# Kernel optimization log

Hardware: AMD Instinct MI355X
Metric: run time of the kernel (lower is better)

## Reference

```python
import jax, jax.numpy as jnp
import numpy as np

N = 100000
E = 1600000
D_IN = 128
D_OUT = 128
NEG_SLOPE = 0.01  # PyTorch LeakyReLU default


def setup_inputs() -> dict:
    key = jax.random.key(0)
    ks = jax.random.split(key, 6)
    x = jax.random.normal(ks[0], (N, D_IN), dtype=jnp.float32)
    src = jax.random.randint(ks[1], (E,), 0, N, dtype=jnp.int32)
    dst = jax.random.randint(ks[2], (E,), 0, N, dtype=jnp.int32)
    e_attn = jax.random.uniform(ks[3], (E,), dtype=jnp.float32)
    # Xavier-normal-ish init for linear weights
    std = float(np.sqrt(2.0 / (D_IN + D_OUT)))
    W1 = jax.random.normal(ks[4], (D_OUT, D_IN), dtype=jnp.float32) * std
    W2 = jax.random.normal(ks[5], (D_OUT, D_IN), dtype=jnp.float32) * std
    b1 = jnp.zeros((D_OUT,), dtype=jnp.float32)
    b2 = jnp.zeros((D_OUT,), dtype=jnp.float32)
    return {"x": x, "src": src, "dst": dst, "e_attn": e_attn,
            "W1": W1, "b1": b1, "W2": W2, "b2": b2}


def leaky_relu(v):
    return jnp.where(v >= 0, v, NEG_SLOPE * v)


def reference(x, src, dst, e_attn, W1, b1, W2, b2):
    # Edge-weighted gather-scatter: h_n[d] = sum_{e: dst(e)=d} a_e * x[src(e)]
    msgs = x[src] * e_attn[:, None]                      # [E, D_IN]
    h_n = jax.ops.segment_sum(msgs, dst, num_segments=N)  # [N, D_IN]
    # Bi-interaction: LeakyReLU(W1(x + h_n)) + LeakyReLU(W2(x * h_n))
    add_part = leaky_relu(jnp.einsum('nd,od->no', x + h_n, W1) + b1)
    mul_part = leaky_relu(jnp.einsum('nd,od->no', x * h_n, W2) + b2)
    return add_part + mul_part  # dropout p=0.0 -> identity
```

## Files before the change

### kernel.cpp

```cpp
#include <hip/hip_runtime.h>

#define N_NODES 100000
#define E_EDGES 1600000
#define D 128
#define AP 132
#define ASTR 136

typedef short s16x8 __attribute__((ext_vector_type(8)));
typedef unsigned short u16x8 __attribute__((ext_vector_type(8)));
typedef float f32x4 __attribute__((ext_vector_type(4)));

__device__ __forceinline__ unsigned short f2bf(float f) {
    union { float f; unsigned u; } v;
    v.f = f;
    unsigned r = v.u + 0x7FFFu + ((v.u >> 16) & 1u);
    return (unsigned short)(r >> 16);
}

__device__ __forceinline__ float bf2f(unsigned short u) {
    union { unsigned u; float f; } v;
    v.u = ((unsigned)u) << 16;
    return v.f;
}

__device__ __forceinline__ float lrelu(float v) {
    return v >= 0.0f ? v : 0.01f * v;
}

__global__ __launch_bounds__(256) void prep_kernel(
    const int* __restrict__ dst, const int* __restrict__ src,
    const float* __restrict__ ea,
    int* __restrict__ cnt, int stride,
    unsigned char* __restrict__ rank, int2* __restrict__ bucket, int cap,
    const float* __restrict__ x, unsigned short* __restrict__ xbf, int do_xconv,
    const float* __restrict__ W1, const float* __restrict__ W2,
    unsigned short* __restrict__ Wswz) {
    int b = blockIdx.x;
    int t = threadIdx.x;
    if (b < 6250) {
        int e = b * 256 + t;
        int d = dst[e];
        if (cap) {
            int s = src[e];
            float a = ea[e];
            int r = atomicAdd(&cnt[(size_t)d * stride], 1);
            if (r < cap) bucket[(size_t)d * cap + r] = make_int2(s, __float_as_int(a));
        } else {
            rank[e] = (unsigned char)atomicAdd(&cnt[(size_t)d * stride], 1);
        }
    } else if (b < 12500) {
        if (!do_xconv) return;
        int idx = (b - 6250) * 256 + t;
        const float4* xp = (const float4*)(x) + (size_t)idx * 2;
        float4 a = xp[0], bb = xp[1];
        u16x8 o;
        o[0] = f2bf(a.x);  o[1] = f2bf(a.y);  o[2] = f2bf(a.z);  o[3] = f2bf(a.w);
        o[4] = f2bf(bb.x); o[5] = f2bf(bb.y); o[6] = f2bf(bb.z); o[7] = f2bf(bb.w);
        ((u16x8*)(xbf))[idx] = o;
    } else {
        int tid = (b - 12500) * 256 + t;
        if (tid >= 2 * 4 * 8 * 64) return;
        int lane = tid & 63;
        int ct   = (tid >> 6) & 7;
        int ks   = (tid >> 9) & 3;
        int mat  = tid >> 11;
        const float* W = mat ? W2 : W1;
        int o  = ct * 16 + (lane & 15);
        int k0 = ks * 32 + (lane >> 4) * 8;
        const float* sp = W + (size_t)o * D + k0;
        u16x8 w;
#pragma unroll
        for (int j = 0; j < 8; ++j) w[j] = f2bf(sp[j]);
        ((u16x8*)(Wswz))[tid] = w;
    }
}

__global__ __launch_bounds__(256) void scanA_kernel(
    const int* __restrict__ cnt, int* __restrict__ excl,
    int* __restrict__ bsum, int n, int stride) {
    __shared__ int tmp[256];
    int gid = blockIdx.x * 256 + threadIdx.x;
    int v = (gid < n) ? cnt[(size_t)gid * stride] : 0;
    tmp[threadIdx.x] = v;
    __syncthreads();
    for (int ofs = 1; ofs < 256; ofs <<= 1) {
        int t = (threadIdx.x >= ofs) ? tmp[threadIdx.x - ofs] : 0;
        __syncthreads();
        tmp[threadIdx.x] += t;
        __syncthreads();
    }
    int incl = tmp[threadIdx.x];
    if (gid < n) excl[gid] = incl - v;
    if (threadIdx.x == 255) bsum[blockIdx.x] = incl;
}

__global__ __launch_bounds__(512) void scanB_kernel(int* __restrict__ bsum, int nb) {
    __shared__ int tmp[512];
    int v = (threadIdx.x < nb) ? bsum[threadIdx.x] : 0;
    tmp[threadIdx.x] = v;
    __syncthreads();
    for (int ofs = 1; ofs < 512; ofs <<= 1) {
        int t = (threadIdx.x >= ofs) ? tmp[threadIdx.x - ofs] : 0;
        __syncthreads();
        tmp[threadIdx.x] += t;
        __syncthreads();
    }
    if (threadIdx.x < nb) bsum[threadIdx.x] = tmp[threadIdx.x] - v;
}

__global__ __launch_bounds__(256) void fillC_kernel(
    const int* __restrict__ src, const int* __restrict__ dst,
    const float* __restrict__ ea, const int* __restrict__ excl,
    const int* __restrict__ bsum, const unsigned char* __restrict__ rank,
    int2* __restrict__ csr, int* __restrict__ off) {
    int gid = blockIdx.x * 256 + threadIdx.x;
    int d = dst[gid];
    int pos = excl[d] + bsum[d >> 8] + (int)rank[gid];
    csr[pos] = make_int2(src[gid], __float_as_int(ea[gid]));
    if (gid < N_NODES) off[gid] = excl[gid] + bsum[gid >> 8];
    else if (gid == N_NODES) off[N_NODES] = E_EDGES;
}

template <bool PADDED>
__global__ __launch_bounds__(256, 4) void fused_gg_kernel(
    const unsigned short* __restrict__ xbf, const int2* __restrict__ csr,
    const int* __restrict__ offc, int stride, int cap,
    const unsigned short* __restrict__ Wswz,
    const float* __restrict__ b1, const float* __restrict__ b2,
    float* __restrict__ out) {
    __shared__ unsigned short A[2][64 * ASTR];

    const int n0 = blockIdx.x * 64;
    const int t = threadIdx.x;
    const int lane = t & 63;
    const int wv = t >> 6;
    const int q = lane >> 4;
    const int li = lane & 15;

    for (int j = 0; j < 16; ++j) {
        const int row = wv * 16 + j;
        const int node = n0 + row;
        int beg = 0, end = 0;
        if (node < N_NODES) {
            if (PADDED) {
                beg = node * cap;
                int c = offc[(size_t)node * stride];
                end = beg + (c < cap ? c : cap);
            } else {
                beg = offc[node];
                end = offc[node + 1];
            }
        }

        float a0[8], a1[8];
#pragma unroll
        for (int d = 0; d < 8; ++d) { a0[d] = 0.f; a1[d] = 0.f; }

        int i = beg + q;
        for (; i + 4 < end; i += 8) {
            int2 p0 = csr[i];
            int2 p1 = csr[i + 4];
            float w0 = __int_as_float(p0.y);
            float w1 = __int_as_float(p1.y);
            u16x8 v0 = ((const u16x8*)(xbf + (size_t)p0.x * D))[li];
            u16x8 v1 = ((const u16x8*)(xbf + (size_t)p1.x * D))[li];
#pragma unroll
            for (int d = 0; d < 8; ++d) {
                a0[d] += w0 * bf2f(v0[d]);
                a1[d] += w1 * bf2f(v1[d]);
            }
        }
        if (i < end) {
            int2 p0 = csr[i];
            float w0 = __int_as_float(p0.y);
            u16x8 v0 = ((const u16x8*)(xbf + (size_t)p0.x * D))[li];
#pragma unroll
            for (int d = 0; d < 8; ++d) a0[d] += w0 * bf2f(v0[d]);
        }
#pragma unroll
        for (int d = 0; d < 8; ++d) a0[d] += a1[d];
#pragma unroll
        for (int d = 0; d < 8; ++d) a0[d] += __shfl_xor(a0[d], 16);
#pragma unroll
        for (int d = 0; d < 8; ++d) a0[d] += __shfl_xor(a0[d], 32);

        const int srcrow = node < N_NODES ? node : N_NODES - 1;
        if (q < 2) {
            u16x8 xu = ((const u16x8*)(xbf + (size_t)srcrow * D))[li];
            u16x8 o;
#pragma unroll
            for (int dd = 0; dd < 8; ++dd) {
                float xv = bf2f(xu[dd]);
                o[dd] = f2bf(q == 0 ? xv + a0[dd] : xv * a0[dd]);
            }
            *(u16x8*)&A[q][row * ASTR + li * 8] = o;
        }
    }

    s16x8 Bf[2][2][4];
    float bb1[2], bb2[2];
#pragma unroll
    for (int ci = 0; ci < 2; ++ci) {
        int ct = wv + ci * 4;
        bb1[ci] = b1[ct * 16 + li];
        bb2[ci] = b2[ct * 16 + li];
#pragma unroll
        for (int mat = 0; mat < 2; ++mat)
#pragma unroll
            for (int ks = 0; ks < 4; ++ks)
                Bf[ci][mat][ks] = *(const s16x8*)(
                    Wswz + ((size_t)(((mat * 4 + ks) * 8 + ct) * 64 + lane)) * 8);
    }

    __syncthreads();

    const int kq = q * 8;
#pragma unroll
    for (int mt = 0; mt < 4; ++mt) {
        f32x4 acc[2][2];
#pragma unroll
        for (int ci = 0; ci < 2; ++ci)
#pragma unroll
            for (int p = 0; p < 2; ++p) acc[ci][p] = (f32x4){0.f, 0.f, 0.f, 0.f};

        const int arow = mt * 16 + li;
#pragma unroll
        for (int ks = 0; ks < 4; ++ks) {
            s16x8 aa0 = *(const s16x8*)&A[0][arow * ASTR + ks * 32 + kq];
            s16x8 aa1 = *(const s16x8*)&A[1][arow * ASTR + ks * 32 + kq];
#pragma unroll
            for (int ci = 0; ci < 2; ++ci) {
                acc[ci][0] = __builtin_amdgcn_mfma_f32_16x16x32_bf16(
                    aa0, Bf[ci][0][ks], acc[ci][0], 0, 0, 0);
                acc[ci][1] = __builtin_amdgcn_mfma_f32_16x16x32_bf16(
                    aa1, Bf[ci][1][ks], acc[ci][1], 0, 0, 0);
            }
        }

#pragma unroll
        for (int ci = 0; ci < 2; ++ci) {
            int oc = (wv + ci * 4) * 16 + li;
#pragma unroll
            for (int r = 0; r < 4; ++r) {
                int node = n0 + mt * 16 + q * 4 + r;
                if (node < N_NODES) {
                    float v = lrelu(acc[ci][0][r] + bb1[ci])
                            + lrelu(acc[ci][1][r] + bb2[ci]);
                    out[(size_t)node * D + oc] = v;
                }
            }
        }
    }
}

__global__ __launch_bounds__(256) void gather_f32_kernel(
    const float* __restrict__ x, const int2* __restrict__ csr,
    const int* __restrict__ off, float* __restrict__ h) {
    int node = blockIdx.x * 4 + (threadIdx.x >> 6);
    int lane = threadIdx.x & 63;
    int beg = off[node];
    int end = off[node + 1];
    float2 acc0 = make_float2(0.f, 0.f);
    float2 acc1 = make_float2(0.f, 0.f);
    int e = beg;
    for (; e + 1 < end; e += 2) {
        int2 p0 = csr[e];
        int2 p1 = csr[e + 1];
        float a0 = __int_as_float(p0.y);
        float a1 = __int_as_float(p1.y);
        float2 v0 = ((const float2*)(x + (size_t)p0.x * D))[lane];
        float2 v1 = ((const float2*)(x + (size_t)p1.x * D))[lane];
        acc0.x += a0 * v0.x; acc0.y += a0 * v0.y;
        acc1.x += a1 * v1.x; acc1.y += a1 * v1.y;
    }
    if (e < end) {
        int2 p0 = csr[e];
        float a0 = __int_as_float(p0.y);
        float2 v0 = ((const float2*)(x + (size_t)p0.x * D))[lane];
        acc0.x += a0 * v0.x; acc0.y += a0 * v0.y;
    }
    acc0.x += acc1.x; acc0.y += acc1.y;
    ((float2*)(h + (size_t)node * D))[lane] = acc0;
}

__global__ __launch_bounds__(256, 4) void mfma_gemm_t1_kernel(
    const float* __restrict__ xf, const float* __restrict__ h,
    const unsigned short* __restrict__ Wswz,
    const float* __restrict__ b1, const float* __restrict__ b2,
    float* __restrict__ out) {
    __shared__ unsigned short A[2][64 * ASTR];
    const int n0 = blockIdx.x * 64;
    const int t = threadIdx.x;
    const int lane = t & 63;
    const int wv = t >> 6;
#pragma unroll
    for (int i = 0; i < 8; ++i) {
        int s = t + i * 256;
        int row = s >> 5;
        int c4 = s & 31;
        int srcrow = n0 + row;
        if (srcrow >= N_NODES) srcrow = N_NODES - 1;
        float4 xv = ((const float4*)(xf + (size_t)srcrow * D))[c4];
        float4 hv = ((const float4*)(h + (size_t)srcrow * D))[c4];
        ushort4 av, mv;
        av.x = f2bf(xv.x + hv.x); av.y = f2bf(xv.y + hv.y);
        av.z = f2bf(xv.z + hv.z); av.w = f2bf(xv.w + hv.w);
        mv.x = f2bf(xv.x * hv.x); mv.y = f2bf(xv.y * hv.y);
        mv.z = f2bf(xv.z * hv.z); mv.w = f2bf(xv.w * hv.w);
        *(ushort4*)&A[0][row * ASTR + c4 * 4] = av;
        *(ushort4*)&A[1][row * ASTR + c4 * 4] = mv;
    }
    s16x8 Bf[2][2][4];
    float bb1[2], bb2[2];
#pragma unroll
    for (int ci = 0; ci < 2; ++ci) {
        int ct = wv + ci * 4;
        bb1[ci] = b1[ct * 16 + (lane & 15)];
        bb2[ci] = b2[ct * 16 + (lane & 15)];
#pragma unroll
        for (int mat = 0; mat < 2; ++mat)
#pragma unroll
            for (int ks = 0; ks < 4; ++ks)
                Bf[ci][mat][ks] = *(const s16x8*)(
                    Wswz + ((size_t)(((mat * 4 + ks) * 8 + ct) * 64 + lane)) * 8);
    }
    __syncthreads();
    const int quad = lane >> 4;
    const int kq = quad * 8;
#pragma unroll
    for (int mt = 0; mt < 4; ++mt) {
        f32x4 acc[2][2];
#pragma unroll
        for (int ci = 0; ci < 2; ++ci)
#pragma unroll
            for (int p = 0; p < 2; ++p) acc[ci][p] = (f32x4){0.f, 0.f, 0.f, 0.f};
        const int arow = mt * 16 + (lane & 15);
#pragma unroll
        for (int ks = 0; ks < 4; ++ks) {
            s16x8 aa0 = *(const s16x8*)&A[0][arow * ASTR + ks * 32 + kq];
            s16x8 aa1 = *(const s16x8*)&A[1][arow * ASTR + ks * 32 + kq];
#pragma unroll
            for (int ci = 0; ci < 2; ++ci) {
                acc[ci][0] = __builtin_amdgcn_mfma_f32_16x16x32_bf16(
                    aa0, Bf[ci][0][ks], acc[ci][0], 0, 0, 0);
                acc[ci][1] = __builtin_amdgcn_mfma_f32_16x16x32_bf16(
                    aa1, Bf[ci][1][ks], acc[ci][1], 0, 0, 0);
            }
        }
#pragma unroll
        for (int ci = 0; ci < 2; ++ci) {
            int oc = (wv + ci * 4) * 16 + (lane & 15);
#pragma unroll
            for (int r = 0; r < 4; ++r) {
                int node = n0 + mt * 16 + quad * 4 + r;
                if (node < N_NODES) {
                    float v = lrelu(acc[ci][0][r] + bb1[ci])
                            + lrelu(acc[ci][1][r] + bb2[ci]);
                    out[(size_t)node * D + oc] = v;
                }
            }
        }
    }
}

__global__ __launch_bounds__(256) void scatter_kernel(
    const float* __restrict__ x, const int* __restrict__ src,
    const int* __restrict__ dst, const float* __restrict__ ea,
    float* __restrict__ h, int E) {
    int idx = blockIdx.x * 256 + threadIdx.x;
    int e = idx >> 5;
    int lane = idx & 31;
    if (e >= E) return;
    int s = src[e];
    int d = dst[e];
    float a = ea[e];
    float4 v = ((const float4*)(x + (size_t)s * D))[lane];
    float* hp = h + (size_t)d * D + lane * 4;
    atomicAdd(hp + 0, a * v.x);
    atomicAdd(hp + 1, a * v.y);
    atomicAdd(hp + 2, a * v.z);
    atomicAdd(hp + 3, a * v.w);
}

__global__ __launch_bounds__(256) void gemm_kernel(
    const float* __restrict__ x, const float* __restrict__ h,
    const float* __restrict__ W1, const float* __restrict__ b1,
    const float* __restrict__ W2, const float* __restrict__ b2,
    float* __restrict__ out) {
    __shared__ float Aadd[32 * AP];
    __shared__ float Amul[32 * AP];
    const int n0 = blockIdx.x * 32;
    const int t = threadIdx.x;
#pragma unroll
    for (int i = 0; i < 4; ++i) {
        int fi = t + i * 256;
        int row = fi >> 5;
        int c4 = fi & 31;
        float4 xv = ((const float4*)(x + (size_t)(n0 + row) * D))[c4];
        float4 hv = ((const float4*)(h + (size_t)(n0 + row) * D))[c4];
        float4 av = make_float4(xv.x + hv.x, xv.y + hv.y, xv.z + hv.z, xv.w + hv.w);
        float4 mv = make_float4(xv.x * hv.x, xv.y * hv.y, xv.z * hv.z, xv.w * hv.w);
        *((float4*)&Aadd[row * AP + c4 * 4]) = av;
        *((float4*)&Amul[row * AP + c4 * 4]) = mv;
    }
    __syncthreads();
    const int m0 = (t >> 5) * 4;
    const int o0 = (t & 31) * 4;
    float acc1[4][4];
    float acc2[4][4];
#pragma unroll
    for (int i = 0; i < 4; ++i)
#pragma unroll
        for (int j = 0; j < 4; ++j) { acc1[i][j] = 0.0f; acc2[i][j] = 0.0f; }
#pragma unroll 4
    for (int d = 0; d < D; d += 4) {
        float4 a[4], m[4], w1[4], w2[4];
#pragma unroll
        for (int i = 0; i < 4; ++i) a[i] = *(const float4*)&Aadd[(m0 + i) * AP + d];
#pragma unroll
        for (int i = 0; i < 4; ++i) m[i] = *(const float4*)&Amul[(m0 + i) * AP + d];
#pragma unroll
        for (int j = 0; j < 4; ++j) w1[j] = *(const float4*)&W1[(size_t)(o0 + j) * D + d];
#pragma unroll
        for (int j = 0; j < 4; ++j) w2[j] = *(const float4*)&W2[(size_t)(o0 + j) * D + d];
#pragma unroll
        for (int i = 0; i < 4; ++i)
#pragma unroll
            for (int j = 0; j < 4; ++j) {
                acc1[i][j] += a[i].x * w1[j].x + a[i].y * w1[j].y
                            + a[i].z * w1[j].z + a[i].w * w1[j].w;
                acc2[i][j] += m[i].x * w2[j].x + m[i].y * w2[j].y
                            + m[i].z * w2[j].z + m[i].w * w2[j].w;
            }
    }
#pragma unroll
    for (int i = 0; i < 4; ++i) {
        float4 r;
        float v1, v2;
        v1 = lrelu(acc1[i][0] + b1[o0 + 0]); v2 = lrelu(acc2[i][0] + b2[o0 + 0]); r.x = v1 + v2;
        v1 = lrelu(acc1[i][1] + b1[o0 + 1]); v2 = lrelu(acc2[i][1] + b2[o0 + 1]); r.y = v1 + v2;
        v1 = lrelu(acc1[i][2] + b1[o0 + 2]); v2 = lrelu(acc2[i][2] + b2[o0 + 2]); r.z = v1 + v2;
        v1 = lrelu(acc1[i][3] + b1[o0 + 3]); v2 = lrelu(acc2[i][3] + b2[o0 + 3]); r.w = v1 + v2;
        ((float4*)(out + (size_t)(n0 + m0 + i) * D))[t & 31] = r;
    }
}

extern "C" void kernel_launch(void* const* d_in, const int* in_sizes, int n_in,
                              void* d_out, int out_size, void* d_ws, size_t ws_size,
                              hipStream_t stream) {
    const float* x   = (const float*)d_in[0];
    const int*   src = (const int*)d_in[1];
    const int*   dst = (const int*)d_in[2];
    const float* ea  = (const float*)d_in[3];
    const float* W1  = (const float*)d_in[4];
    const float* b1  = (const float*)d_in[5];
    const float* W2  = (const float*)d_in[6];
    const float* b2  = (const float*)d_in[7];
    float* out = (float*)d_out;
    char* ws = (char*)d_ws;

    auto align256 = [](size_t v) { return (v + 255) & ~(size_t)255; };

    const size_t SZ_WSWZ = 2 * 4 * 8 * 64 * 8 * sizeof(unsigned short);
    const size_t SZ_OFF  = (size_t)(N_NODES + 1) * sizeof(int);
    const size_t SZ_EXCL = (size_t)N_NODES * sizeof(int);
    const size_t SZ_BSUM = 512 * sizeof(int);
    const size_t SZ_RANK = (size_t)E_EDGES;
    const size_t SZ_CSR  = (size_t)E_EDGES * sizeof(int2);
    const size_t SZ_XBF  = (size_t)N_NODES * D * sizeof(unsigned short);

    const int NB_E = 6250;
    const int NB_N = (N_NODES + 255) / 256;
    const int GB   = (N_NODES + 63) / 64;

    auto try_direct = [&](int cap) -> bool {
        size_t sz_cnt = (size_t)N_NODES * 16 * sizeof(int);
        size_t o_cnt  = align256(SZ_WSWZ);
        size_t o_bkt  = o_cnt + align256(sz_cnt);
        size_t o_xbf  = o_bkt + align256((size_t)N_NODES * cap * sizeof(int2));
        size_t need   = o_xbf + align256(SZ_XBF);
        if (ws_size < need) return false;
        unsigned short* Wswz = (unsigned short*)ws;
        int*  cnt = (int*)(ws + o_cnt);
        int2* bkt = (int2*)(ws + o_bkt);
        unsigned short* xbf = (unsigned short*)(ws + o_xbf);
        hipMemsetAsync(cnt, 0, sz_cnt, stream);
        prep_kernel<<<12516, 256, 0, stream>>>(dst, src, ea, cnt, 16,
                                               nullptr, bkt, cap,
                                               x, xbf, 1, W1, W2, Wswz);
        fused_gg_kernel<true><<<GB, 256, 0, stream>>>(xbf, bkt, cnt, 16, cap,
                                                      Wswz, b1, b2, out);
        return true;
    };
    if (try_direct(64)) return;
    if (try_direct(48)) return;

    auto try_exact = [&](int stride) -> bool {
        size_t sz_cnt = (size_t)N_NODES * stride * sizeof(int);
        size_t o_cnt  = align256(SZ_WSWZ);
        size_t o_off  = o_cnt + align256(sz_cnt);
        size_t o_excl = o_off + align256(SZ_OFF);
        size_t o_bsum = o_excl + align256(SZ_EXCL);
        size_t o_rank = o_bsum + align256(SZ_BSUM);
        size_t o_csr  = o_rank + align256(SZ_RANK);
        size_t o_xbf  = o_csr + align256(SZ_CSR);
        size_t need   = o_xbf + align256(SZ_XBF);
        if (ws_size < need) return false;
        unsigned short* Wswz = (unsigned short*)ws;
        int*  cnt  = (int*)(ws + o_cnt);
        int*  off  = (int*)(ws + o_off);
        int*  excl = (int*)(ws + o_excl);
        int*  bsum = (int*)(ws + o_bsum);
        unsigned char* rank = (unsigned char*)(ws + o_rank);
        int2* csr  = (int2*)(ws + o_csr);
        unsigned short* xbf = (unsigned short*)(ws + o_xbf);
        hipMemsetAsync(cnt, 0, sz_cnt, stream);
        prep_kernel<<<12516, 256, 0, stream>>>(dst, src, ea, cnt, stride,
                                               rank, nullptr, 0,
                                               x, xbf, 1, W1, W2, Wswz);
        scanA_kernel<<<NB_N, 256, 0, stream>>>(cnt, excl, bsum, N_NODES, stride);
        scanB_kernel<<<1, 512, 0, stream>>>(bsum, NB_N);
        fillC_kernel<<<NB_E, 256, 0, stream>>>(src, dst, ea, excl, bsum, rank,
                                               csr, off);
        fused_gg_kernel<false><<<GB, 256, 0, stream>>>(xbf, csr, off, 0, 0,
                                                       Wswz, b1, b2, out);
        return true;
    };
    if (try_exact(16)) return;
    if (try_exact(1)) return;

    {
        size_t sz_cnt = (size_t)N_NODES * sizeof(int);
        size_t o_cnt  = align256(SZ_WSWZ);
        size_t o_off  = o_cnt + align256(sz_cnt);
        size_t o_excl = o_off + align256(SZ_OFF);
        size_t o_bsum = o_excl + align256(SZ_EXCL);
        size_t o_rank = o_bsum + align256(SZ_BSUM);
        size_t o_csr  = o_rank + align256(SZ_RANK);
        size_t need   = o_csr + align256(SZ_CSR);
        if (ws_size >= need) {
            unsigned short* Wswz = (unsigned short*)ws;
            int*  cnt  = (int*)(ws + o_cnt);
            int*  off  = (int*)(ws + o_off);
            int*  excl = (int*)(ws + o_excl);
            int*  bsum = (int*)(ws + o_bsum);
            unsigned char* rank = (unsigned char*)(ws + o_rank);
            int2* csr  = (int2*)(ws + o_csr);
            hipMemsetAsync(cnt, 0, sz_cnt, stream);
            prep_kernel<<<12516, 256, 0, stream>>>(dst, src, ea, cnt, 1,
                                                   rank, nullptr, 0,
                                                   x, nullptr, 0, W1, W2, Wswz);
            scanA_kernel<<<NB_N, 256, 0, stream>>>(cnt, excl, bsum, N_NODES, 1);
            scanB_kernel<<<1, 512, 0, stream>>>(bsum, NB_N);
            fillC_kernel<<<NB_E, 256, 0, stream>>>(src, dst, ea, excl, bsum, rank,
                                                   csr, off);
            float* h = out;
            gather_f32_kernel<<<N_NODES / 4, 256, 0, stream>>>(x, csr, off, h);
            mfma_gemm_t1_kernel<<<GB, 256, 0, stream>>>(x, h, Wswz, b1, b2, out);
            return;
        }
    }

    {
        float* h = out;
        hipMemsetAsync(h, 0, (size_t)N_NODES * D * sizeof(float), stream);
        int total = E_EDGES * 32;
        scatter_kernel<<<(total + 255) / 256, 256, 0, stream>>>(x, src, dst, ea,
                                                                h, E_EDGES);
        gemm_kernel<<<N_NODES / 32, 256, 0, stream>>>(x, h, W1, b1, W2, b2, out);
    }
}
```

Baseline: 311.9 us.

## Drop padded-bucket direct path, use exact CSR with 4-way unrolled gather

```diff
diff --git a/kernel.cpp b/kernel.cpp
--- a/kernel.cpp
+++ b/kernel.cpp
@@ -28,10 +28,8 @@
 }
 
 __global__ __launch_bounds__(256) void prep_kernel(
-    const int* __restrict__ dst, const int* __restrict__ src,
-    const float* __restrict__ ea,
-    int* __restrict__ cnt, int stride,
-    unsigned char* __restrict__ rank, int2* __restrict__ bucket, int cap,
+    const int* __restrict__ dst, int* __restrict__ cnt,
+    unsigned char* __restrict__ rank, int stride,
     const float* __restrict__ x, unsigned short* __restrict__ xbf, int do_xconv,
     const float* __restrict__ W1, const float* __restrict__ W2,
     unsigned short* __restrict__ Wswz) {
@@ -39,15 +37,7 @@
     int t = threadIdx.x;
     if (b < 6250) {
         int e = b * 256 + t;
-        int d = dst[e];
-        if (cap) {
-            int s = src[e];
-            float a = ea[e];
-            int r = atomicAdd(&cnt[(size_t)d * stride], 1);
-            if (r < cap) bucket[(size_t)d * cap + r] = make_int2(s, __float_as_int(a));
-        } else {
-            rank[e] = (unsigned char)atomicAdd(&cnt[(size_t)d * stride], 1);
-        }
+        rank[e] = (unsigned char)atomicAdd(&cnt[(size_t)dst[e] * stride], 1);
     } else if (b < 12500) {
         if (!do_xconv) return;
         int idx = (b - 6250) * 256 + t;
@@ -121,10 +111,9 @@
     else if (gid == N_NODES) off[N_NODES] = E_EDGES;
 }
 
-template <bool PADDED>
 __global__ __launch_bounds__(256, 4) void fused_gg_kernel(
     const unsigned short* __restrict__ xbf, const int2* __restrict__ csr,
-    const int* __restrict__ offc, int stride, int cap,
+    const int* __restrict__ off,
     const unsigned short* __restrict__ Wswz,
     const float* __restrict__ b1, const float* __restrict__ b2,
     float* __restrict__ out) {
@@ -142,35 +131,37 @@
         const int node = n0 + row;
         int beg = 0, end = 0;
         if (node < N_NODES) {
-            if (PADDED) {
-                beg = node * cap;
-                int c = offc[(size_t)node * stride];
-                end = beg + (c < cap ? c : cap);
-            } else {
-                beg = offc[node];
-                end = offc[node + 1];
-            }
-        }
-
-        float a0[8], a1[8];
-#pragma unroll
-        for (int d = 0; d < 8; ++d) { a0[d] = 0.f; a1[d] = 0.f; }
+            beg = off[node];
+            end = off[node + 1];
+        }
+
+        float a0[8], a1[8], a2[8], a3[8];
+#pragma unroll
+        for (int d = 0; d < 8; ++d) { a0[d] = 0.f; a1[d] = 0.f; a2[d] = 0.f; a3[d] = 0.f; }
 
         int i = beg + q;
-        for (; i + 4 < end; i += 8) {
+        for (; i + 12 < end; i += 16) {
             int2 p0 = csr[i];
             int2 p1 = csr[i + 4];
+            int2 p2 = csr[i + 8];
+            int2 p3 = csr[i + 12];
             float w0 = __int_as_float(p0.y);
             float w1 = __int_as_float(p1.y);
+            float w2 = __int_as_float(p2.y);
+            float w3 = __int_as_float(p3.y);
             u16x8 v0 = ((const u16x8*)(xbf + (size_t)p0.x * D))[li];
             u16x8 v1 = ((const u16x8*)(xbf + (size_t)p1.x * D))[li];
+            u16x8 v2 = ((const u16x8*)(xbf + (size_t)p2.x * D))[li];
+            u16x8 v3 = ((const u16x8*)(xbf + (size_t)p3.x * D))[li];
 #pragma unroll
             for (int d = 0; d < 8; ++d) {
                 a0[d] += w0 * bf2f(v0[d]);
                 a1[d] += w1 * bf2f(v1[d]);
-            }
-        }
-        if (i < end) {
+                a2[d] += w2 * bf2f(v2[d]);
+                a3[d] += w3 * bf2f(v3[d]);
+            }
+        }
+        for (; i < end; i += 4) {
             int2 p0 = csr[i];
             float w0 = __int_as_float(p0.y);
             u16x8 v0 = ((const u16x8*)(xbf + (size_t)p0.x * D))[li];
@@ -178,7 +169,7 @@
             for (int d = 0; d < 8; ++d) a0[d] += w0 * bf2f(v0[d]);
         }
 #pragma unroll
-        for (int d = 0; d < 8; ++d) a0[d] += a1[d];
+        for (int d = 0; d < 8; ++d) a0[d] += a1[d] + a2[d] + a3[d];
 #pragma unroll
         for (int d = 0; d < 8; ++d) a0[d] += __shfl_xor(a0[d], 16);
 #pragma unroll
@@ -472,28 +463,6 @@
     const int NB_E = 6250;
     const int NB_N = (N_NODES + 255) / 256;
     const int GB   = (N_NODES + 63) / 64;
-
-    auto try_direct = [&](int cap) -> bool {
-        size_t sz_cnt = (size_t)N_NODES * 16 * sizeof(int);
-        size_t o_cnt  = align256(SZ_WSWZ);
-        size_t o_bkt  = o_cnt + align256(sz_cnt);
-        size_t o_xbf  = o_bkt + align256((size_t)N_NODES * cap * sizeof(int2));
-        size_t need   = o_xbf + align256(SZ_XBF);
-        if (ws_size < need) return false;
-        unsigned short* Wswz = (unsigned short*)ws;
-        int*  cnt = (int*)(ws + o_cnt);
-        int2* bkt = (int2*)(ws + o_bkt);
-        unsigned short* xbf = (unsigned short*)(ws + o_xbf);
-        hipMemsetAsync(cnt, 0, sz_cnt, stream);
-        prep_kernel<<<12516, 256, 0, stream>>>(dst, src, ea, cnt, 16,
-                                               nullptr, bkt, cap,
-                                               x, xbf, 1, W1, W2, Wswz);
-        fused_gg_kernel<true><<<GB, 256, 0, stream>>>(xbf, bkt, cnt, 16, cap,
-                                                      Wswz, b1, b2, out);
-        return true;
-    };
-    if (try_direct(64)) return;
-    if (try_direct(48)) return;
 
     auto try_exact = [&](int stride) -> bool {
         size_t sz_cnt = (size_t)N_NODES * stride * sizeof(int);
@@ -515,15 +484,13 @@
         int2* csr  = (int2*)(ws + o_csr);
         unsigned short* xbf = (unsigned short*)(ws + o_xbf);
         hipMemsetAsync(cnt, 0, sz_cnt, stream);
-        prep_kernel<<<12516, 256, 0, stream>>>(dst, src, ea, cnt, stride,
-                                               rank, nullptr, 0,
+        prep_kernel<<<12516, 256, 0, stream>>>(dst, cnt, rank, stride,
                                                x, xbf, 1, W1, W2, Wswz);
         scanA_kernel<<<NB_N, 256, 0, stream>>>(cnt, excl, bsum, N_NODES, stride);
         scanB_kernel<<<1, 512, 0, stream>>>(bsum, NB_N);
         fillC_kernel<<<NB_E, 256, 0, stream>>>(src, dst, ea, excl, bsum, rank,
                                                csr, off);
-        fused_gg_kernel<false><<<GB, 256, 0, stream>>>(xbf, csr, off, 0, 0,
-                                                       Wswz, b1, b2, out);
+        fused_gg_kernel<<<GB, 256, 0, stream>>>(xbf, csr, off, Wswz, b1, b2, out);
         return true;
     };
     if (try_exact(16)) return;
@@ -547,8 +514,7 @@
             unsigned char* rank = (unsigned char*)(ws + o_rank);
             int2* csr  = (int2*)(ws + o_csr);
             hipMemsetAsync(cnt, 0, sz_cnt, stream);
-            prep_kernel<<<12516, 256, 0, stream>>>(dst, src, ea, cnt, 1,
-                                                   rank, nullptr, 0,
+            prep_kernel<<<12516, 256, 0, stream>>>(dst, cnt, rank, 1,
                                                    x, nullptr, 0, W1, W2, Wswz);
             scanA_kernel<<<NB_N, 256, 0, stream>>>(cnt, excl, bsum, N_NODES, 1);
             scanB_kernel<<<1, 512, 0, stream>>>(bsum, NB_N);
```

Result: slower. 337.6 us (+8.2%).
